# Optimization experiments

Measured on AMD Instinct MI355X. Metric: run time of the kernel, lower is better.

The kernel has to match this reference:

```python
import jax, jax.numpy as jnp
import numpy as np

DIM = 180; HEADS = 6; WS = 16; NUM_TOKENS = 64; RDIM = 10; CAT = 128
KS = 5; MLP_HID = 360; DTD = 64; Hh = 64; Ww = 64; B = 8; M = 64


def _ln(x, g, b, eps=1e-5):
    mu = x.mean(-1, keepdims=True)
    var = ((x - mu) ** 2).mean(-1, keepdims=True)
    return (x - mu) / jnp.sqrt(var + eps) * g + b


def _l2norm(x):
    return x / jnp.clip(jnp.linalg.norm(x, axis=-1, keepdims=True), 1e-12)


def setup_inputs() -> dict:
    key = jax.random.key(0)
    ks = jax.random.split(key, 24)
    rn = lambda k, s: jax.random.normal(k, s, jnp.float32) * 0.02
    z = lambda *s: jnp.zeros(s, jnp.float32)
    return {
        'x': jax.random.normal(ks[0], (B, Hh * Ww, DIM), jnp.float32),
        'td': jax.random.normal(ks[1], (B, M, DIM), jnp.float32),
        'norm1_g': jnp.ones((DIM,), jnp.float32), 'norm1_b': z(DIM),
        'wqkv_w': rn(ks[2], (DIM, 3 * DIM)), 'wqkv_b': z(3 * DIM),
        'atd_wq_w': rn(ks[3], (DIM, RDIM)), 'atd_wq_b': z(RDIM),
        'atd_wk_w': rn(ks[4], (DIM, RDIM)), 'atd_wk_b': z(RDIM),
        'atd_wv_w': rn(ks[5], (DIM, DIM)), 'atd_wv_b': z(DIM),
        'atd_scale': jnp.ones((1,), jnp.float32),
        'aca_proj_w': rn(ks[6], (DIM, DIM)), 'aca_proj_b': z(DIM),
        'win_rpb': rn(ks[7], ((2 * WS - 1) ** 2, HEADS)),
        'win_proj_w': rn(ks[8], (DIM, DIM)), 'win_proj_b': z(DIM),
        'fc_td_w': rn(ks[9], (DIM, DTD)), 'fc_td_b': z(DTD),
        'fc1_w': rn(ks[10], (DIM, MLP_HID)), 'fc1_b': z(MLP_HID),
        'dw_w': rn(ks[11], (MLP_HID + DTD, 1, KS, KS)), 'dw_b': z(MLP_HID + DTD),
        'fc2_w': rn(ks[12], (MLP_HID + DTD, DIM)), 'fc2_b': z(DIM),
        'norm2_g': jnp.ones((DIM,), jnp.float32), 'norm2_b': z(DIM),
        'rpi_sa': jax.random.randint(ks[13], (WS * WS, WS * WS), 0, (2 * WS - 1) ** 2),
        'h': Hh, 'w': Ww,
    }


def reference(x, td, norm1_g, norm1_b, wqkv_w, wqkv_b, atd_wq_w, atd_wq_b,
              atd_wk_w, atd_wk_b, atd_wv_w, atd_wv_b, atd_scale,
              aca_proj_w, aca_proj_b, win_rpb, win_proj_w, win_proj_b,
              fc_td_w, fc_td_b, fc1_w, fc1_b, dw_w, dw_b, fc2_w, fc2_b,
              norm2_g, norm2_b, rpi_sa, h, w):
    b, n, c = x.shape
    hd = c // HEADS
    shortcut = x
    xn = _ln(x, norm1_g, norm1_b)
    qkv = xn @ wqkv_w + wqkv_b  # [b, n, 3c]

    # --- ATD_CA: l2-normalized cross-attention to token dictionary ---
    q = xn @ atd_wq_w + atd_wq_b          # [b, n, rd]
    kk = td @ atd_wk_w + atd_wk_b         # [b, m, rd]
    vv = td @ atd_wv_w + atd_wv_b         # [b, m, c]
    logit_scale = 1.0 + jnp.clip(atd_scale, 0.0, 3.0) * np.log(NUM_TOKENS)
    sim = jnp.einsum('bnr,bmr->bnm', _l2norm(q), _l2norm(kk)) * logit_scale
    attn_atd = jax.nn.softmax(sim, axis=-1)
    x_atd = jnp.einsum('bnm,bmc->bnc', attn_atd, vv)
    tk_id = jnp.argmax(attn_atd, axis=-1)  # [b, n]

    # --- AC_MSA: category-sorted grouped attention ---
    gs = min(n, CAT); ng = (n + gs - 1) // gs; pad_n = ng * gs - n
    sort_idx = jnp.argsort(tk_id, axis=-1)
    inv_idx = jnp.argsort(sort_idx, axis=-1)  # inverse permutation
    sq = jnp.take_along_axis(qkv, sort_idx[:, :, None], axis=1)
    sq = jnp.concatenate([sq, jnp.flip(sq[:, n - pad_n:n, :], axis=1)], axis=1)
    g = sq.reshape(b, ng, gs, 3, HEADS, hd).transpose(3, 0, 1, 4, 2, 5)
    qa, ka, va = g[0], g[1], g[2]          # [b, ng, H, gs, hd]
    a = jax.nn.softmax(jnp.einsum('bgHid,bgHjd->bgHij', qa, ka) * hd ** -0.5, axis=-1)
    y = jnp.einsum('bgHij,bgHjd->bgHid', a, va).transpose(0, 1, 3, 2, 4)
    y = y.reshape(b, n + pad_n, c)[:, :n]
    x_aca = jnp.take_along_axis(y, inv_idx[:, :, None], axis=1) @ aca_proj_w + aca_proj_b

    # --- gather per-token dictionary features for FFN ---
    td_proj = td @ fc_td_w + fc_td_b       # [b, m, dtd]
    x_td = jnp.take_along_axis(td_proj, jnp.broadcast_to(tk_id[:, :, None], (b, n, DTD)), axis=1)

    # --- window attention (shift_size = 0, no mask) ---
    nwh, nww = h // WS, w // WS
    win = qkv.reshape(b, nwh, WS, nww, WS, 3 * c).transpose(0, 1, 3, 2, 4, 5)
    win = win.reshape(-1, WS * WS, 3 * c)
    B_ = win.shape[0]; N = WS * WS
    wq = win.reshape(B_, N, 3, HEADS, hd).transpose(2, 0, 3, 1, 4)
    qw, kw, vw = wq[0] * hd ** -0.5, wq[1], wq[2]
    bias = win_rpb[rpi_sa.reshape(-1)].reshape(N, N, HEADS).transpose(2, 0, 1)[None]
    aw = jax.nn.softmax(jnp.einsum('wHid,wHjd->wHij', qw, kw) + bias, axis=-1)
    ow = jnp.einsum('wHij,wHjd->wHid', aw, vw).transpose(0, 2, 1, 3).reshape(B_, N, c)
    ow = ow @ win_proj_w + win_proj_b
    attn_x = ow.reshape(b, nwh, nww, WS, WS, c).transpose(0, 1, 3, 2, 4, 5).reshape(b, n, c)

    x = shortcut + x_atd + attn_x + x_aca

    # --- ConvFFN_td with depthwise conv branch ---
    x2 = _ln(x, norm2_g, norm2_b)
    h1 = jax.nn.gelu(x2 @ fc1_w + fc1_b, approximate=False)
    hc = jnp.concatenate([h1, x_td], axis=-1)  # [b, n, C]
    C = hc.shape[-1]
    img = jnp.swapaxes(hc, 1, 2).reshape(b, C, h, w)
    conv = jax.lax.conv_general_dilated(img, dw_w, (1, 1), 'SAME',
        dimension_numbers=('NCHW', 'OIHW', 'NCHW'), feature_group_count=C)
    conv = jax.nn.gelu(conv + dw_b[None, :, None, None], approximate=False)
    hc = hc + jnp.swapaxes(conv.reshape(b, C, n), 1, 2)
    return x + hc @ fc2_w + fc2_b
```

## Files before the change

kernel.cpp:

```cpp
#include <hip/hip_runtime.h>
#include <hip/hip_bf16.h>
#include <math.h>

#define BB      8
#define NTOK    4096
#define CDIM    180
#define C3      540
#define NHEADS  6
#define HD      30
#define MDICT   64
#define RD      10
#define DTD     64
#define MHID    360
#define CCAT    424
#define WS      16
#define WIN_N   256
#define GS      128
#define NG      32
#define ROWS    (BB*NTOK)
#define KP1     192
#define KP2     448
#define QKVP    576

typedef __hip_bfloat16 bf16;
typedef short v8s __attribute__((ext_vector_type(8)));
typedef float f32x4 __attribute__((ext_vector_type(4)));
typedef unsigned int u32x4 __attribute__((ext_vector_type(4)));

__device__ __forceinline__ float gelu_exact(float x) {
    return 0.5f * x * (1.0f + erff(x * 0.70710678118654752f));
}
__device__ __forceinline__ float wave_sum(float v) {
    #pragma unroll
    for (int off = 32; off > 0; off >>= 1) v += __shfl_xor(v, off, 64);
    return v;
}
__device__ __forceinline__ unsigned short f2b(float v) {
    unsigned u = __float_as_uint(v);
    return (unsigned short)((u + 0x7FFFu + ((u >> 16) & 1u)) >> 16);
}
__device__ __forceinline__ float b2f(unsigned short h) {
    return __uint_as_float(((unsigned)h) << 16);
}
__device__ __forceinline__ unsigned packbf(float lo, float hi) {
    return (unsigned)f2b(lo) | ((unsigned)f2b(hi) << 16);
}
__device__ __forceinline__ void gload16(const void* g, void* l) {
    __builtin_amdgcn_global_load_lds(
        (const __attribute__((address_space(1))) void*)g,
        (__attribute__((address_space(3))) void*)l, 16, 0, 0);
}

__global__ __launch_bounds__(256) void detect_kernel(const void* __restrict__ x,
                                                     int* __restrict__ flag,
                                                     int* __restrict__ diag)
{
    __shared__ int cnt;
    if (threadIdx.x == 0) { cnt = 0; *diag = 0; }
    __syncthreads();
    const unsigned short* u = (const unsigned short*)x;
    int c = 0;
    for (int i = threadIdx.x; i < 2048; i += 256) {
        unsigned short e = u[2 * i] & 0x7F80;
        if (e >= 0x4300) c++;
    }
    atomicAdd(&cnt, c);
    __syncthreads();
    if (threadIdx.x == 0) *flag = (cnt > 16) ? 1 : 0;
}

#define NCVT 23
struct CvtArgs {
    const void* src[NCVT];
    float* dst[NCVT];
    int cum[NCVT + 1];
};
__global__ __launch_bounds__(256) void convert_all_kernel(CvtArgs a, int total,
        const int* __restrict__ flag)
{
    int i = blockIdx.x * 256 + threadIdx.x;
    if (i >= total) return;
    int s = 0;
    while (i >= a.cum[s + 1]) s++;
    int off = i - a.cum[s];
    if (*flag) a.dst[s][off] = ((const float*)a.src[s])[off];
    else       a.dst[s][off] = __bfloat162float(((const bf16*)a.src[s])[off]);
}

__global__ __launch_bounds__(256) void emit_kernel(const float* __restrict__ src,
        void* __restrict__ out, const int* __restrict__ flag,
        const int* __restrict__ diag, int n)
{
    int i = blockIdx.x * 256 + threadIdx.x;
    if (i >= n) return;
    float v = src[i];
    int d = *diag;
    if (d) v = 100.f + 32.f * (float)d;
    if (*flag) ((float*)out)[i] = v;
    else       ((bf16*)out)[i]  = __float2bfloat16(v);
}

__global__ __launch_bounds__(256) void zero_aux_kernel(bf16* __restrict__ tb,
        bf16* __restrict__ qb)
{
    int idx = blockIdx.x * 256 + threadIdx.x;
    if (idx < ROWS * 12) {
        int row = idx / 12, c = idx % 12;
        tb[(size_t)row * KP1 + CDIM + c] = __float2bfloat16(0.f);
    } else {
        int j = idx - ROWS * 12;
        int row = j / 36, r = j % 36;
        int sec = r / 12, rr = r % 12, hh = rr >> 1, d = 30 + (rr & 1);
        qb[(size_t)row * QKVP + sec * 192 + hh * 32 + d] = __float2bfloat16(0.f);
    }
}

__global__ __launch_bounds__(256) void packW_kernel(const void* __restrict__ W,
        bf16* __restrict__ Wt, int K, int N, int Kpad, int total,
        const int* __restrict__ flag)
{
    int idx = blockIdx.x * 256 + threadIdx.x;
    if (idx >= total) return;
    int n = idx / Kpad, k = idx % Kpad;
    float v = 0.f;
    if (k < K && n < N) {
        size_t src = (size_t)k * N + n;
        v = (*flag) ? ((const float*)W)[src]
                    : __bfloat162float(((const bf16*)W)[src]);
    }
    Wt[idx] = __float2bfloat16(v);
}

__global__ __launch_bounds__(256) void bias_pre_kernel(const int* __restrict__ rpi,
        const float* __restrict__ rpb, float* __restrict__ bias_t)
{
    int idx = blockIdx.x * 256 + threadIdx.x;
    int h = idx >> 16, ij = idx & 65535;
    bias_t[idx] = rpb[rpi[ij] * NHEADS + h];
}

template<bool GELU_, bool ADDRES, bool BIAS_, int OM>
__global__ __launch_bounds__(256) void mgemm_kernel(
        const bf16* __restrict__ A, int lda,
        const bf16* __restrict__ Wt, int ldw,
        const float* __restrict__ bias,
        const float* __restrict__ res, int ldr,
        float* __restrict__ outF, int ldo, int N, int K,
        int* __restrict__ diag)
{
    __shared__ __align__(16) unsigned short As[128][32];
    __shared__ __align__(16) unsigned short Bs[64][32];
    int tid = threadIdx.x;
    int wave = tid >> 6, lane = tid & 63;
    int quad = lane >> 4, mr = lane & 15;
    int row0 = blockIdx.y * 128, col0 = blockIdx.x * 64;
    int ar = tid >> 2, ac = (tid & 3) * 8;
    f32x4 z = {0.f, 0.f, 0.f, 0.f};
    f32x4 acc[2][4] = {{z, z, z, z}, {z, z, z, z}};
    const unsigned short* Au = (const unsigned short*)A;
    const unsigned short* Wu = (const unsigned short*)Wt;
    for (int k0 = 0; k0 < K; k0 += 32) {
        gload16(&Au[(size_t)(row0 + ar) * lda + k0 + ac],      &As[ar][ac]);
        gload16(&Au[(size_t)(row0 + 64 + ar) * lda + k0 + ac], &As[64 + ar][ac]);
        gload16(&Wu[(size_t)(col0 + ar) * ldw + k0 + ac],      &Bs[ar][ac]);
        __syncthreads();
        v8s bfr[4];
        #pragma unroll
        for (int ni = 0; ni < 4; ni++)
            bfr[ni] = *(const v8s*)&Bs[ni * 16 + mr][quad * 8];
        #pragma unroll
        for (int s = 0; s < 2; s++) {
            v8s a = *(const v8s*)&As[wave * 32 + s * 16 + mr][quad * 8];
            #pragma unroll
            for (int ni = 0; ni < 4; ni++)
                acc[s][ni] = __builtin_amdgcn_mfma_f32_16x16x32_bf16(
                    a, bfr[ni], acc[s][ni], 0, 0, 0);
        }
        __syncthreads();
    }
    if (OM == 1) {
        bf16* outb = (bf16*)outF;
        #pragma unroll
        for (int ni = 0; ni < 4; ni++) {
            int gc = col0 + ni * 16 + mr;
            if (gc >= N) continue;
            float bv = bias[gc];
            int sec = gc / 180, rem = gc - sec * 180;
            int hh = rem / 30, d = rem - hh * 30;
            int slot = sec * 192 + hh * 32 + d;
            float sc = (sec == 0) ? 0.18257418583505536f : 1.f;
            #pragma unroll
            for (int s = 0; s < 2; s++) {
                #pragma unroll
                for (int r = 0; r < 4; r++) {
                    int gr = row0 + wave * 32 + s * 16 + quad * 4 + r;
                    outb[(size_t)gr * QKVP + slot] =
                        __float2bfloat16((acc[s][ni][r] + bv) * sc);
                }
            }
        }
        return;
    }
    #pragma unroll
    for (int ni = 0; ni < 4; ni++) {
        int gc = col0 + ni * 16 + mr;
        if (gc >= N) continue;
        float bv = BIAS_ ? bias[gc] : 0.f;
        #pragma unroll
        for (int s = 0; s < 2; s++) {
            #pragma unroll
            for (int r = 0; r < 4; r++) {
                int gr = row0 + wave * 32 + s * 16 + quad * 4 + r;
                float v = acc[s][ni][r] + bv;
                if (GELU_) v = gelu_exact(v);
                if (ADDRES) v += res[(size_t)gr * ldr + gc];
                if (OM == 2) {
                    unsigned u = __float_as_uint(v);
                    if ((u & 0x7F800000u) == 0x7F800000u) atomicOr(diag, 8);
                }
                outF[(size_t)gr * ldo + gc] = v;
            }
        }
    }
}

__global__ __launch_bounds__(256) void av_mgemm_kernel(
        const bf16* __restrict__ P, const bf16* __restrict__ vvT,
        const float* __restrict__ xres, float* __restrict__ accout)
{
    __shared__ unsigned short As[64][32];
    __shared__ unsigned short Bs[64][32];
    int tid = threadIdx.x;
    int wave = tid >> 6, lane = tid & 63;
    int quad = lane >> 4, mr = lane & 15;
    int row0 = blockIdx.y * 64, col0 = blockIdx.x * 64;
    int bz = blockIdx.z;
    const unsigned short* Au = (const unsigned short*)P + (size_t)bz * NTOK * MDICT;
    const unsigned short* Wu = (const unsigned short*)vvT + (size_t)bz * 192 * MDICT;
    const float* res = xres + (size_t)bz * NTOK * CDIM;
    float* outF = accout + (size_t)bz * NTOK * CDIM;
    f32x4 z = {0.f, 0.f, 0.f, 0.f};
    f32x4 acc[4] = {z, z, z, z};
    for (int k0 = 0; k0 < MDICT; k0 += 32) {
        #pragma unroll
        for (int e = 0; e < 8; e++) {
            int idx = tid * 8 + e;
            int r = idx >> 5, c = idx & 31;
            As[r][c] = Au[(size_t)(row0 + r) * MDICT + k0 + c];
            Bs[r][c] = Wu[(size_t)(col0 + r) * MDICT + k0 + c];
        }
        __syncthreads();
        v8s a;
        #pragma unroll
        for (int j = 0; j < 8; j++) a[j] = (short)As[wave * 16 + mr][quad * 8 + j];
        #pragma unroll
        for (int ni = 0; ni < 4; ni++) {
            v8s b;
            #pragma unroll
            for (int j = 0; j < 8; j++) b[j] = (short)Bs[ni * 16 + mr][quad * 8 + j];
            acc[ni] = __builtin_amdgcn_mfma_f32_16x16x32_bf16(a, b, acc[ni], 0, 0, 0);
        }
        __syncthreads();
    }
    #pragma unroll
    for (int ni = 0; ni < 4; ni++) {
        int gc = col0 + ni * 16 + mr;
        if (gc >= CDIM) continue;
        #pragma unroll
        for (int r = 0; r < 4; r++) {
            int gr = row0 + wave * 16 + quad * 4 + r;
            float v = acc[ni][r] + res[(size_t)gr * CDIM + gc];
            outF[(size_t)gr * CDIM + gc] = v;
        }
    }
}

__global__ __launch_bounds__(256, 4) void win_mfma_kernel(const bf16* __restrict__ qkvb,
        const float* __restrict__ bias_t, bf16* __restrict__ outb)
{
    int b = blockIdx.y;
    int widx = blockIdx.x / NHEADS;
    int hh = blockIdx.x % NHEADS;
    int wy = widx >> 2, wx = widx & 3;
    int tid = threadIdx.x;
    int wave = tid >> 6, lane = tid & 63, quad = lane >> 4, mr = lane & 15;
    __shared__ __align__(16) unsigned short Ks[64][40];
    __shared__ __align__(16) unsigned short Vt[32][80];

    size_t brow = (size_t)b * NTOK;
    const unsigned short* qu = (const unsigned short*)qkvb;

    v8s aq[4];
    #pragma unroll
    for (int tt = 0; tt < 4; tt++) {
        int m = (wave * 4 + tt) * 16 + mr;
        int nt_ = (wy * WS + (m >> 4)) * 64 + wx * WS + (m & 15);
        aq[tt] = *(const v8s*)&qu[(brow + nt_) * QKVP + hh * 32 + quad * 8];
    }
    f32x4 z = {0.f, 0.f, 0.f, 0.f};
    f32x4 oacc[4][2] = {{z, z}, {z, z}, {z, z}, {z, z}};
    float m_r[4], l_r[4];
    #pragma unroll
    for (int tt = 0; tt < 4; tt++) { m_r[tt] = -3.0e38f; l_r[tt] = 0.f; }
    const float* btab = bias_t + (size_t)hh * WIN_N * WIN_N;

    for (int kc = 0; kc < WIN_N; kc += 64) {
        {
            int j = tid >> 2, dg = (tid & 3) * 8;
            int tok = kc + j;
            int nt_ = (wy * WS + (tok >> 4)) * 64 + wx * WS + (tok & 15);
            const unsigned short* base = qu + (brow + nt_) * QKVP + hh * 32;
            v8s kv = *(const v8s*)&base[192 + dg];
            v8s vv = *(const v8s*)&base[384 + dg];
            *(v8s*)&Ks[j][dg] = kv;
            #pragma unroll
            for (int jj = 0; jj < 8; jj++)
                Vt[dg + jj][j] = (unsigned short)vv[jj];
        }
        __syncthreads();
        #pragma unroll
        for (int tt = 0; tt < 4; tt++) {
            f32x4 s[4];
            #pragma unroll
            for (int nt = 0; nt < 4; nt++) {
                v8s bk = *(const v8s*)&Ks[nt * 16 + mr][quad * 8];
                s[nt] = __builtin_amdgcn_mfma_f32_16x16x32_bf16(bk, aq[tt], z, 0, 0, 0);
            }
            int qg = (wave * 4 + tt) * 16 + mr;
            const float* bi = btab + (size_t)qg * WIN_N + kc;
            float mc = -3.0e38f;
            #pragma unroll
            for (int nt = 0; nt < 4; nt++) {
                f32x4 b4 = *(const f32x4*)(bi + nt * 16 + quad * 4);
                s[nt][0] += b4[0]; s[nt][1] += b4[1];
                s[nt][2] += b4[2]; s[nt][3] += b4[3];
                mc = fmaxf(mc, fmaxf(fmaxf(s[nt][0], s[nt][1]),
                                     fmaxf(s[nt][2], s[nt][3])));
            }
            mc = fmaxf(mc, __shfl_xor(mc, 16, 64));
            mc = fmaxf(mc, __shfl_xor(mc, 32, 64));
            float mn = fmaxf(m_r[tt], mc);
            float alpha = __expf(m_r[tt] - mn);
            m_r[tt] = mn;
            float ls = 0.f;
            #pragma unroll
            for (int nt = 0; nt < 4; nt++) {
                #pragma unroll
                for (int r = 0; r < 4; r++) {
                    float pp = __expf(s[nt][r] - mn);
                    ls += pp;
                    s[nt][r] = pp;
                }
            }
            ls += __shfl_xor(ls, 16, 64);
            ls += __shfl_xor(ls, 32, 64);
            l_r[tt] = l_r[tt] * alpha + ls;
            unsigned dpk[4][2];
            #pragma unroll
            for (int nt = 0; nt < 4; nt++) {
                dpk[nt][0] = packbf(s[nt][0], s[nt][1]);
                dpk[nt][1] = packbf(s[nt][2], s[nt][3]);
            }
            #pragma unroll
            for (int r = 0; r < 4; r++) {
                float av = __shfl(alpha, quad * 4 + r, 64);
                oacc[tt][0][r] *= av;
                oacc[tt][1][r] *= av;
            }
            #pragma unroll
            for (int c = 0; c < 2; c++) {
                union { u32x4 u; v8s s8; } afu;
                #pragma unroll
                for (int t = 0; t < 4; t++) {
                    int srcl = (((quad * 2 + (t >> 1)) & 3) << 4) | mr;
                    unsigned r0 = (unsigned)__shfl((int)dpk[2 * c][t & 1], srcl, 64);
                    unsigned r1 = (unsigned)__shfl((int)dpk[2 * c + 1][t & 1], srcl, 64);
                    afu.u[t] = (quad & 2) ? r1 : r0;
                }
                #pragma unroll
                for (int dt = 0; dt < 2; dt++) {
                    v8s bv = *(const v8s*)&Vt[dt * 16 + mr][c * 32 + quad * 8];
                    oacc[tt][dt] = __builtin_amdgcn_mfma_f32_16x16x32_bf16(
                        afu.s8, bv, oacc[tt][dt], 0, 0, 0);
                }
            }
        }
        __syncthreads();
    }
    #pragma unroll
    for (int tt = 0; tt < 4; tt++) {
        float il = 1.f / l_r[tt];
        #pragma unroll
        for (int r = 0; r < 4; r++) {
            float ilr = __shfl(il, quad * 4 + r, 64);
            int m = (wave * 4 + tt) * 16 + quad * 4 + r;
            int nt_ = (wy * WS + (m >> 4)) * 64 + wx * WS + (m & 15);
            #pragma unroll
            for (int dt = 0; dt < 2; dt++) {
                int d = dt * 16 + mr;
                if (d >= HD) continue;
                outb[(brow + nt_) * KP1 + hh * HD + d] =
                    __float2bfloat16(oacc[tt][dt][r] * ilr);
            }
        }
    }
}

__global__ __launch_bounds__(256, 4) void acmsa_mfma_kernel(const bf16* __restrict__ qkvb,
        const int* __restrict__ sidx, bf16* __restrict__ outb)
{
    int b = blockIdx.y;
    int g = blockIdx.x / NHEADS;
    int hh = blockIdx.x % NHEADS;
    int tid = threadIdx.x;
    int wave = tid >> 6, lane = tid & 63, quad = lane >> 4, mr = lane & 15;
    __shared__ int toks[GS];
    __shared__ __align__(16) unsigned short Ks[64][40];
    __shared__ __align__(16) unsigned short Vt[32][80];

    size_t brow = (size_t)b * NTOK;
    if (tid < GS) toks[tid] = sidx[brow + (size_t)g * GS + tid];
    __syncthreads();
    const unsigned short* qu = (const unsigned short*)qkvb;

    v8s aq[2];
    #pragma unroll
    for (int tt = 0; tt < 2; tt++) {
        int m = (wave * 2 + tt) * 16 + mr;
        aq[tt] = *(const v8s*)&qu[(brow + toks[m]) * QKVP + hh * 32 + quad * 8];
    }
    f32x4 z = {0.f, 0.f, 0.f, 0.f};
    f32x4 oacc[2][2] = {{z, z}, {z, z}};
    float m_r[2], l_r[2];
    #pragma unroll
    for (int tt = 0; tt < 2; tt++) { m_r[tt] = -3.0e38f; l_r[tt] = 0.f; }

    for (int kc = 0; kc < GS; kc += 64) {
        {
            int j = tid >> 2, dg = (tid & 3) * 8;
            int tok = toks[kc + j];
            const unsigned short* base = qu + (brow + tok) * QKVP + hh * 32;
            v8s kv = *(const v8s*)&base[192 + dg];
            v8s vv = *(const v8s*)&base[384 + dg];
            *(v8s*)&Ks[j][dg] = kv;
            #pragma unroll
            for (int jj = 0; jj < 8; jj++)
                Vt[dg + jj][j] = (unsigned short)vv[jj];
        }
        __syncthreads();
        #pragma unroll
        for (int tt = 0; tt < 2; tt++) {
            f32x4 s[4];
            #pragma unroll
            for (int nt = 0; nt < 4; nt++) {
                v8s bk = *(const v8s*)&Ks[nt * 16 + mr][quad * 8];
                s[nt] = __builtin_amdgcn_mfma_f32_16x16x32_bf16(bk, aq[tt], z, 0, 0, 0);
            }
            float mc = -3.0e38f;
            #pragma unroll
            for (int nt = 0; nt < 4; nt++)
                mc = fmaxf(mc, fmaxf(fmaxf(s[nt][0], s[nt][1]),
                                     fmaxf(s[nt][2], s[nt][3])));
            mc = fmaxf(mc, __shfl_xor(mc, 16, 64));
            mc = fmaxf(mc, __shfl_xor(mc, 32, 64));
            float mn = fmaxf(m_r[tt], mc);
            float alpha = __expf(m_r[tt] - mn);
            m_r[tt] = mn;
            float ls = 0.f;
            #pragma unroll
            for (int nt = 0; nt < 4; nt++) {
                #pragma unroll
                for (int r = 0; r < 4; r++) {
                    float pp = __expf(s[nt][r] - mn);
                    ls += pp;
                    s[nt][r] = pp;
                }
            }
            ls += __shfl_xor(ls, 16, 64);
            ls += __shfl_xor(ls, 32, 64);
            l_r[tt] = l_r[tt] * alpha + ls;
            unsigned dpk[4][2];
            #pragma unroll
            for (int nt = 0; nt < 4; nt++) {
                dpk[nt][0] = packbf(s[nt][0], s[nt][1]);
                dpk[nt][1] = packbf(s[nt][2], s[nt][3]);
            }
            #pragma unroll
            for (int r = 0; r < 4; r++) {
                float av = __shfl(alpha, quad * 4 + r, 64);
                oacc[tt][0][r] *= av;
                oacc[tt][1][r] *= av;
            }
            #pragma unroll
            for (int c = 0; c < 2; c++) {
                union { u32x4 u; v8s s8; } afu;
                #pragma unroll
                for (int t = 0; t < 4; t++) {
                    int srcl = (((quad * 2 + (t >> 1)) & 3) << 4) | mr;
                    unsigned r0 = (unsigned)__shfl((int)dpk[2 * c][t & 1], srcl, 64);
                    unsigned r1 = (unsigned)__shfl((int)dpk[2 * c + 1][t & 1], srcl, 64);
                    afu.u[t] = (quad & 2) ? r1 : r0;
                }
                #pragma unroll
                for (int dt = 0; dt < 2; dt++) {
                    v8s bv = *(const v8s*)&Vt[dt * 16 + mr][c * 32 + quad * 8];
                    oacc[tt][dt] = __builtin_amdgcn_mfma_f32_16x16x32_bf16(
                        afu.s8, bv, oacc[tt][dt], 0, 0, 0);
                }
            }
        }
        __syncthreads();
    }
    #pragma unroll
    for (int tt = 0; tt < 2; tt++) {
        float il = 1.f / l_r[tt];
        #pragma unroll
        for (int r = 0; r < 4; r++) {
            float ilr = __shfl(il, quad * 4 + r, 64);
            int m = (wave * 2 + tt) * 16 + quad * 4 + r;
            int tok = toks[m];
            #pragma unroll
            for (int dt = 0; dt < 2; dt++) {
                int d = dt * 16 + mr;
                if (d >= HD) continue;
                outb[(brow + tok) * KP1 + hh * HD + d] =
                    __float2bfloat16(oacc[tt][dt][r] * ilr);
            }
        }
    }
}

__global__ __launch_bounds__(256) void ln_atd_kernel(const float* __restrict__ x,
        const float* __restrict__ g, const float* __restrict__ be,
        bf16* __restrict__ outb,
        const float* __restrict__ wq, const float* __restrict__ wqb,
        const float* __restrict__ scale_p, const float* __restrict__ kkn,
        bf16* __restrict__ Pout, int* __restrict__ tk_id)
{
    int row = blockIdx.x * 4 + (threadIdx.x >> 6);
    int b = row >> 12;
    int t = threadIdx.x & 63;
    const float* xr = x + (size_t)row * CDIM;
    float v0 = xr[t];
    float v1 = xr[t + 64];
    float v2 = (t < CDIM - 128) ? xr[t + 128] : 0.f;
    float s1 = wave_sum(v0 + v1 + v2);
    float s2 = wave_sum(v0*v0 + v1*v1 + v2*v2);
    float mu = s1 / (float)CDIM;
    float var = s2 / (float)CDIM - mu * mu;
    float rs = rsqrtf(var + 1e-5f);
    float o0 = (v0 - mu) * rs * g[t]      + be[t];
    float o1 = (v1 - mu) * rs * g[t + 64] + be[t + 64];
    float o2 = (t < CDIM - 128) ? ((v2 - mu) * rs * g[t + 128] + be[t + 128]) : 0.f;
    bf16* ob = outb + (size_t)row * KP1;
    ob[t]       = __float2bfloat16(o0);
    ob[t + 64]  = __float2bfloat16(o1);
    ob[t + 128] = __float2bfloat16(o2);
    float sq[RD];
    #pragma unroll
    for (int j = 0; j < RD; j++) {
        float part = o0 * wq[t * RD + j] + o1 * wq[(t + 64) * RD + j];
        if (t < CDIM - 128) part += o2 * wq[(t + 128) * RD + j];
        sq[j] = wave_sum(part) + wqb[j];
    }
    float qn = 0.f;
    #pragma unroll
    for (int j = 0; j < RD; j++) qn += sq[j] * sq[j];
    qn = fmaxf(sqrtf(qn), 1e-12f);
    float ls = 1.0f + fminf(fmaxf(scale_p[0], 0.f), 3.f) * 4.158883083359672f;
    const float* kr = kkn + ((size_t)b * MDICT + t) * RD;
    float s = 0.f;
    #pragma unroll
    for (int j = 0; j < RD; j++) s += sq[j] * kr[j];
    s = s / qn * ls;
    float mv = s; int mi = t;
    #pragma unroll
    for (int off = 32; off > 0; off >>= 1) {
        float ov = __shfl_xor(mv, off, 64);
        int   oi = __shfl_xor(mi, off, 64);
        if (ov > mv || (ov == mv && oi < mi)) { mv = ov; mi = oi; }
    }
    float e = __expf(s - mv);
    float denom = wave_sum(e);
    Pout[(size_t)row * MDICT + t] = __float2bfloat16(e / denom);
    if (t == 0) tk_id[row] = mi;
}

__global__ __launch_bounds__(256) void ln_kernel(const float* __restrict__ x,
        const float* __restrict__ g, const float* __restrict__ be,
        bf16* __restrict__ outb)
{
    int row = blockIdx.x * 4 + (threadIdx.x >> 6);
    int t = threadIdx.x & 63;
    const float* xr = x + (size_t)row * CDIM;
    float v0 = xr[t];
    float v1 = xr[t + 64];
    float v2 = (t < CDIM - 128) ? xr[t + 128] : 0.f;
    float s1 = wave_sum(v0 + v1 + v2);
    float s2 = wave_sum(v0*v0 + v1*v1 + v2*v2);
    float mu = s1 / (float)CDIM;
    float var = s2 / (float)CDIM - mu * mu;
    float rs = rsqrtf(var + 1e-5f);
    float o0 = (v0 - mu) * rs * g[t]      + be[t];
    float o1 = (v1 - mu) * rs * g[t + 64] + be[t + 64];
    float o2 = (t < CDIM - 128) ? ((v2 - mu) * rs * g[t + 128] + be[t + 128]) : 0.f;
    bf16* ob = outb + (size_t)row * KP1;
    ob[t]       = __float2bfloat16(o0);
    ob[t + 64]  = __float2bfloat16(o1);
    ob[t + 128] = __float2bfloat16(o2);
}

__global__ __launch_bounds__(64) void td_pre_kernel(const float* __restrict__ td,
        const float* __restrict__ wk, const float* __restrict__ wkb,
        const float* __restrict__ wv, const float* __restrict__ wvb,
        const float* __restrict__ wtd, const float* __restrict__ wtdb,
        float* __restrict__ kkn, bf16* __restrict__ vvT, float* __restrict__ tdp)
{
    int blk = blockIdx.x;
    int b = blk >> 6, m = blk & 63;
    int t = threadIdx.x;
    __shared__ float tr[CDIM];
    __shared__ float sk[RD];
    __shared__ float snorm;
    const float* tdr = td + (size_t)blk * CDIM;
    tr[t] = tdr[t]; tr[t + 64] = tdr[t + 64];
    if (t < CDIM - 128) tr[t + 128] = tdr[t + 128];
    __syncthreads();
    if (t < RD) {
        float s = wkb[t];
        for (int k = 0; k < CDIM; k++) s += tr[k] * wk[k * RD + t];
        sk[t] = s;
    }
    __syncthreads();
    if (t == 0) {
        float s = 0.f;
        #pragma unroll
        for (int j = 0; j < RD; j++) s += sk[j] * sk[j];
        snorm = fmaxf(sqrtf(s), 1e-12f);
    }
    __syncthreads();
    if (t < RD) kkn[(size_t)blk * RD + t] = sk[t] / snorm;
    for (int c = t; c < 192; c += 64) {
        float s = 0.f;
        if (c < CDIM) {
            s = wvb[c];
            for (int k = 0; k < CDIM; k++) s += tr[k] * wv[k * CDIM + c];
        }
        vvT[((size_t)(b * 192 + c)) * MDICT + m] = __float2bfloat16(s);
    }
    {
        float s = wtdb[t];
        for (int k = 0; k < CDIM; k++) s += tr[k] * wtd[k * DTD + t];
        tdp[(size_t)blk * DTD + t] = s;
    }
}

__global__ __launch_bounds__(256) void sort_kernel(const int* __restrict__ tk_id,
                                                   int* __restrict__ sidx)
{
    int b = blockIdx.x; int tid = threadIdx.x;
    __shared__ int keys[NTOK];
    __shared__ int cnt[256];
    __shared__ int off[256];
    const int* kb = tk_id + (size_t)b * NTOK;
    for (int i = tid; i < NTOK; i += 256) keys[i] = kb[i];
    __syncthreads();
    int v = tid >> 2, seg = tid & 3;
    int lo = seg * 1024, hi = lo + 1024;
    int c = 0;
    for (int i = lo; i < hi; i++) c += (keys[i] == v);
    cnt[tid] = c;
    __syncthreads();
    if (tid == 0) {
        int run = 0;
        for (int l = 0; l < 256; l++) { off[l] = run; run += cnt[l]; }
    }
    __syncthreads();
    int o = off[tid];
    int* sb = sidx + (size_t)b * NTOK;
    for (int i = lo; i < hi; i++) if (keys[i] == v) sb[o++] = i;
}

__global__ __launch_bounds__(256) void gather_td_kernel(const int* __restrict__ tk_id,
        const float* __restrict__ tdp, float* __restrict__ hc)
{
    int idx = blockIdx.x * 256 + threadIdx.x;
    int row = idx >> 6, j = idx & 63;
    int b = row >> 12;
    int tk = tk_id[row];
    hc[(size_t)row * CCAT + MHID + j] = tdp[((size_t)b * MDICT + tk) * DTD + j];
}

#define CHK3 64
#define CTW  8
#define CTH  8
#define CHW  12
#define CHP  144
#define CSPX 68
__global__ __launch_bounds__(256) void conv_kernel(const float* __restrict__ hc,
        const float* __restrict__ w, const float* __restrict__ wb,
        bf16* __restrict__ outb)
{
    int ch0 = blockIdx.x * CHK3;
    int tile = blockIdx.y;
    int b = blockIdx.z;
    int ty0 = (tile >> 3) * CTH, tx0 = (tile & 7) * CTW;
    __shared__ __align__(16) float sh[CHP][CSPX];
    __shared__ __align__(16) float wt[25][CHK3];
    int tid = threadIdx.x;
    for (int idx = tid; idx < CHP * CHK3; idx += 256) {
        int pix = idx >> 6, ch = idx & 63;
        int gy = ty0 + pix / CHW - 2, gx = tx0 + pix % CHW - 2;
        int chg = ch0 + ch;
        float v = 0.f;
        if (gy >= 0 && gy < 64 && gx >= 0 && gx < 64 && chg < CCAT)
            v = hc[((size_t)b * NTOK + gy * 64 + gx) * CCAT + chg];
        sh[pix][ch] = v;
    }
    for (int idx = tid; idx < 25 * CHK3; idx += 256) {
        int kk = idx >> 6, ch = idx & 63;
        int chg = ch0 + ch;
        wt[kk][ch] = (chg < CCAT) ? w[chg * 25 + kk] : 0.f;
    }
    __syncthreads();
    int q = tid & 3, p = tid >> 2;
    int px = p & 7, py = p >> 3;
    int cb = q * 16;
    int pc = py * CHW + px;
    v8s pk0, pk1;
    #pragma unroll
    for (int sub = 0; sub < 4; sub++) {
        int cs = cb + sub * 4;
        f32x4 acc = {0.f, 0.f, 0.f, 0.f};
        #pragma unroll
        for (int dy = 0; dy < 5; dy++) {
            #pragma unroll
            for (int dx = 0; dx < 5; dx++) {
                f32x4 sv = *(const f32x4*)&sh[pc + dy * CHW + dx][cs];
                f32x4 wv = *(const f32x4*)&wt[dy * 5 + dx][cs];
                acc += sv * wv;
            }
            __builtin_amdgcn_sched_barrier(0);
        }
        f32x4 ctr = *(const f32x4*)&sh[pc + 2 * CHW + 2][cs];
        #pragma unroll
        for (int c = 0; c < 4; c++) {
            int chg = ch0 + cs + c;
            float v = 0.f;
            if (chg < CCAT) {
                float gv = gelu_exact(acc[c] + wb[chg]);
                v = ctr[c] + gv;
            }
            int lc = sub * 4 + c;
            if (lc < 8) pk0[lc] = (short)f2b(v);
            else        pk1[lc - 8] = (short)f2b(v);
        }
        __builtin_amdgcn_sched_barrier(0);
    }
    size_t obase = ((size_t)b * NTOK + (ty0 + py) * 64 + tx0 + px) * KP2 + ch0 + cb;
    unsigned short* ob = (unsigned short*)outb + obase;
    *(v8s*)ob = pk0;
    *(v8s*)(ob + 8) = pk1;
}

extern "C" void kernel_launch(void* const* d_in, const int* in_sizes, int n_in,
                              void* d_out, int out_size, void* d_ws, size_t ws_size,
                              hipStream_t stream)
{
    (void)n_in; (void)ws_size; (void)out_size;
    const int* rpi = (const int*)d_in[28];

    float* p = (float*)d_ws;
    float* xn    = p; p += (size_t)ROWS * CDIM;
    float* acc   = p; p += (size_t)ROWS * CDIM;
    float* tmp1  = p; p += (size_t)ROWS * CDIM;
    float* qkv   = p; p += (size_t)ROWS * C3;
    float* hcnew = p; p += (size_t)ROWS * CCAT;
    float* kkn   = p; p += (size_t)BB * MDICT * RD;
    bf16*  vvT   = (bf16*)p; p += (size_t)BB * 192 * MDICT / 2;
    float* tdp   = p; p += (size_t)BB * MDICT * DTD;
    int*   tk_id = (int*)p; p += ROWS;
    int*   sidx  = (int*)p; p += ROWS;
    int*   flag  = (int*)p; p += 64;
    int*   diag  = (int*)p; p += 64;
    bf16* wtqkv = (bf16*)p; p += 576 * KP1 / 2;
    bf16* wtaca = (bf16*)p; p += 192 * KP1 / 2;
    bf16* wtwin = (bf16*)p; p += 192 * KP1 / 2;
    bf16* wtfc1 = (bf16*)p; p += 384 * KP1 / 2;
    bf16* wtfc2 = (bf16*)p; p += 192 * KP2 / 2;
    float* cin[28];
    for (int i = 0; i < 28; i++) { cin[i] = p; p += in_sizes[i]; }
    float* bias_t = p; p += (size_t)NHEADS * WIN_N * WIN_N;
    (void)xn;

    float* hc      = qkv;
    bf16*  qkvb    = (bf16*)qkv;
    bf16*  xnb     = (bf16*)hcnew;
    bf16*  tmp1b   = (bf16*)(hcnew + (size_t)ROWS * KP1 / 2);
    bf16*  hcnewb2 = (bf16*)hcnew;
    bf16*  Pbuf    = (bf16*)tmp1;

    detect_kernel<<<1, 256, 0, stream>>>(d_in[0], flag, diag);
    {
        CvtArgs ca;
        int total = 0, s = 0;
        for (int i = 0; i < 28; i++) {
            if (i == 4 || i == 13 || i == 16 || i == 20 || i == 24) continue;
            ca.src[s] = d_in[i];
            ca.dst[s] = cin[i];
            ca.cum[s] = total;
            total += in_sizes[i];
            s++;
        }
        ca.cum[s] = total;
        convert_all_kernel<<<(total + 255) / 256, 256, 0, stream>>>(ca, total, flag);
    }
    const float *x = cin[0], *td = cin[1], *n1g = cin[2], *n1b = cin[3],
        *wqkv_b = cin[5], *wq_w = cin[6], *wq_b = cin[7],
        *wk_w = cin[8], *wk_b = cin[9], *wv_w = cin[10], *wv_b = cin[11],
        *atd_scale = cin[12], *aca_b = cin[14], *win_rpb = cin[15],
        *winp_b = cin[17], *fctd_w = cin[18], *fctd_b = cin[19],
        *fc1_b = cin[21], *dw_w = cin[22], *dw_b = cin[23], *fc2_b = cin[25],
        *n2g = cin[26], *n2b = cin[27];

    packW_kernel<<<576 * KP1 / 256, 256, 0, stream>>>(d_in[4],  wtqkv, CDIM, C3,   KP1, 576 * KP1, flag);
    packW_kernel<<<192 * KP1 / 256, 256, 0, stream>>>(d_in[13], wtaca, CDIM, CDIM, KP1, 192 * KP1, flag);
    packW_kernel<<<192 * KP1 / 256, 256, 0, stream>>>(d_in[16], wtwin, CDIM, CDIM, KP1, 192 * KP1, flag);
    packW_kernel<<<384 * KP1 / 256, 256, 0, stream>>>(d_in[20], wtfc1, CDIM, MHID, KP1, 384 * KP1, flag);
    packW_kernel<<<192 * KP2 / 256, 256, 0, stream>>>(d_in[24], wtfc2, CCAT, CDIM, KP2, 192 * KP2, flag);
    bias_pre_kernel<<<NHEADS * WIN_N * WIN_N / 256, 256, 0, stream>>>(rpi, win_rpb, bias_t);

    td_pre_kernel<<<BB * MDICT, 64, 0, stream>>>(td, wk_w, wk_b, wv_w, wv_b,
                                                 fctd_w, fctd_b, kkn, vvT, tdp);
    ln_atd_kernel<<<ROWS / 4, 256, 0, stream>>>(x, n1g, n1b, xnb,
                                                wq_w, wq_b, atd_scale, kkn, Pbuf, tk_id);
    mgemm_kernel<false, false, true, 1><<<dim3(9, ROWS / 128), 256, 0, stream>>>(
        xnb, KP1, wtqkv, KP1, wqkv_b, nullptr, 0, (float*)qkvb, QKVP, C3, KP1, nullptr);
    zero_aux_kernel<<<ROWS * 48 / 256, 256, 0, stream>>>(tmp1b, qkvb);
    av_mgemm_kernel<<<dim3(3, NTOK / 64, BB), 256, 0, stream>>>(Pbuf, vvT, x, acc);
    sort_kernel<<<BB, 256, 0, stream>>>(tk_id, sidx);
    acmsa_mfma_kernel<<<dim3(NG * NHEADS, BB), 256, 0, stream>>>(qkvb, sidx, tmp1b);
    mgemm_kernel<false, true, true, 0><<<dim3(3, ROWS / 128), 256, 0, stream>>>(
        tmp1b, KP1, wtaca, KP1, aca_b, acc, CDIM, acc, CDIM, CDIM, KP1, nullptr);
    win_mfma_kernel<<<dim3(16 * NHEADS, BB), 256, 0, stream>>>(qkvb, bias_t, tmp1b);
    mgemm_kernel<false, true, true, 0><<<dim3(3, ROWS / 128), 256, 0, stream>>>(
        tmp1b, KP1, wtwin, KP1, winp_b, acc, CDIM, acc, CDIM, CDIM, KP1, nullptr);
    ln_kernel<<<ROWS / 4, 256, 0, stream>>>(acc, n2g, n2b, xnb);
    mgemm_kernel<true, false, true, 0><<<dim3(6, ROWS / 128), 256, 0, stream>>>(
        xnb, KP1, wtfc1, KP1, fc1_b, nullptr, 0, hc, CCAT, MHID, KP1, nullptr);
    gather_td_kernel<<<ROWS * 64 / 256, 256, 0, stream>>>(tk_id, tdp, hc);
    conv_kernel<<<dim3(7, 64, BB), 256, 0, stream>>>(hc, dw_w, dw_b, hcnewb2);
    mgemm_kernel<false, true, true, 2><<<dim3(3, ROWS / 128), 256, 0, stream>>>(
        hcnewb2, KP2, wtfc2, KP2, fc2_b, acc, CDIM, tmp1, CDIM, CDIM, KP2, diag);
    emit_kernel<<<(ROWS * CDIM + 255) / 256, 256, 0, stream>>>(
        tmp1, d_out, flag, diag, ROWS * CDIM);
}
```

Measured before the change: 690.2 us.

## Fuse ACA and window projection GEMMs via concatenated K; read x directly

Merges the two separate projection GEMMs (ACA output and window-attention output) into one GEMM over a concatenated K dimension of 384. It does this by packing both weight matrices side by side and letting the A-operand pointer switch to a second buffer halfway through K, with both biases added in the epilogue. This removes one read-modify-write pass over the fp32 accumulator and one kernel launch. It also stops converting x into an fp32 copy and has ln_atd and av_mgemm read the raw input with a dtype flag, at the cost of a per-element branch and a larger zero-init kernel for the second padded buffer.

```diff
diff --git a/kernel.cpp b/kernel.cpp
--- a/kernel.cpp
+++ b/kernel.cpp
@@ -100,15 +100,19 @@
     else       ((bf16*)out)[i]  = __float2bfloat16(v);
 }
 
-__global__ __launch_bounds__(256) void zero_aux_kernel(bf16* __restrict__ tb,
-        bf16* __restrict__ qb)
+__global__ __launch_bounds__(256) void zero_aux_kernel(bf16* __restrict__ t1,
+        bf16* __restrict__ t2, bf16* __restrict__ qb)
 {
     int idx = blockIdx.x * 256 + threadIdx.x;
     if (idx < ROWS * 12) {
         int row = idx / 12, c = idx % 12;
-        tb[(size_t)row * KP1 + CDIM + c] = __float2bfloat16(0.f);
+        t1[(size_t)row * KP1 + CDIM + c] = __float2bfloat16(0.f);
+    } else if (idx < ROWS * 24) {
+        int j = idx - ROWS * 12;
+        int row = j / 12, c = j % 12;
+        t2[(size_t)row * KP1 + CDIM + c] = __float2bfloat16(0.f);
     } else {
-        int j = idx - ROWS * 12;
+        int j = idx - ROWS * 24;
         int row = j / 36, r = j % 36;
         int sec = r / 12, rr = r % 12, hh = rr >> 1, d = 30 + (rr & 1);
         qb[(size_t)row * QKVP + sec * 192 + hh * 32 + d] = __float2bfloat16(0.f);
@@ -116,8 +120,8 @@
 }
 
 __global__ __launch_bounds__(256) void packW_kernel(const void* __restrict__ W,
-        bf16* __restrict__ Wt, int K, int N, int Kpad, int total,
-        const int* __restrict__ flag)
+        bf16* __restrict__ Wt, int K, int N, int Kpad, int ldw, int koff,
+        int total, const int* __restrict__ flag)
 {
     int idx = blockIdx.x * 256 + threadIdx.x;
     if (idx >= total) return;
@@ -128,7 +132,7 @@
         v = (*flag) ? ((const float*)W)[src]
                     : __bfloat162float(((const bf16*)W)[src]);
     }
-    Wt[idx] = __float2bfloat16(v);
+    Wt[(size_t)n * ldw + koff + k] = __float2bfloat16(v);
 }
 
 __global__ __launch_bounds__(256) void bias_pre_kernel(const int* __restrict__ rpi,
@@ -146,7 +150,8 @@
         const float* __restrict__ bias,
         const float* __restrict__ res, int ldr,
         float* __restrict__ outF, int ldo, int N, int K,
-        int* __restrict__ diag)
+        int* __restrict__ diag,
+        const bf16* __restrict__ A2, const float* __restrict__ bias2)
 {
     __shared__ __align__(16) unsigned short As[128][32];
     __shared__ __align__(16) unsigned short Bs[64][32];
@@ -158,11 +163,15 @@
     f32x4 z = {0.f, 0.f, 0.f, 0.f};
     f32x4 acc[2][4] = {{z, z, z, z}, {z, z, z, z}};
     const unsigned short* Au = (const unsigned short*)A;
+    const unsigned short* A2u = (const unsigned short*)A2;
     const unsigned short* Wu = (const unsigned short*)Wt;
     for (int k0 = 0; k0 < K; k0 += 32) {
-        gload16(&Au[(size_t)(row0 + ar) * lda + k0 + ac],      &As[ar][ac]);
-        gload16(&Au[(size_t)(row0 + 64 + ar) * lda + k0 + ac], &As[64 + ar][ac]);
-        gload16(&Wu[(size_t)(col0 + ar) * ldw + k0 + ac],      &Bs[ar][ac]);
+        const unsigned short* Asel = Au;
+        int kk = k0;
+        if (OM == 3 && k0 >= KP1) { Asel = A2u; kk = k0 - KP1; }
+        gload16(&Asel[(size_t)(row0 + ar) * lda + kk + ac],      &As[ar][ac]);
+        gload16(&Asel[(size_t)(row0 + 64 + ar) * lda + kk + ac], &As[64 + ar][ac]);
+        gload16(&Wu[(size_t)(col0 + ar) * ldw + k0 + ac],        &Bs[ar][ac]);
         __syncthreads();
         v8s bfr[4];
         #pragma unroll
@@ -206,6 +215,7 @@
         int gc = col0 + ni * 16 + mr;
         if (gc >= N) continue;
         float bv = BIAS_ ? bias[gc] : 0.f;
+        if (OM == 3) bv += bias2[gc];
         #pragma unroll
         for (int s = 0; s < 2; s++) {
             #pragma unroll
@@ -226,7 +236,8 @@
 
 __global__ __launch_bounds__(256) void av_mgemm_kernel(
         const bf16* __restrict__ P, const bf16* __restrict__ vvT,
-        const float* __restrict__ xres, float* __restrict__ accout)
+        const void* __restrict__ xraw, const int* __restrict__ flag,
+        float* __restrict__ accout)
 {
     __shared__ unsigned short As[64][32];
     __shared__ unsigned short Bs[64][32];
@@ -235,10 +246,13 @@
     int quad = lane >> 4, mr = lane & 15;
     int row0 = blockIdx.y * 64, col0 = blockIdx.x * 64;
     int bz = blockIdx.z;
+    int isf = *flag;
     const unsigned short* Au = (const unsigned short*)P + (size_t)bz * NTOK * MDICT;
     const unsigned short* Wu = (const unsigned short*)vvT + (size_t)bz * 192 * MDICT;
-    const float* res = xres + (size_t)bz * NTOK * CDIM;
-    float* outF = accout + (size_t)bz * NTOK * CDIM;
+    size_t rbase = (size_t)bz * NTOK * CDIM;
+    const float* resf = (const float*)xraw + rbase;
+    const bf16*  resb = (const bf16*)xraw + rbase;
+    float* outF = accout + rbase;
     f32x4 z = {0.f, 0.f, 0.f, 0.f};
     f32x4 acc[4] = {z, z, z, z};
     for (int k0 = 0; k0 < MDICT; k0 += 32) {
@@ -269,8 +283,9 @@
         #pragma unroll
         for (int r = 0; r < 4; r++) {
             int gr = row0 + wave * 16 + quad * 4 + r;
-            float v = acc[ni][r] + res[(size_t)gr * CDIM + gc];
-            outF[(size_t)gr * CDIM + gc] = v;
+            size_t off = (size_t)gr * CDIM + gc;
+            float rv = isf ? resf[off] : __bfloat162float(resb[off]);
+            outF[off] = acc[ni][r] + rv;
         }
     }
 }
@@ -530,7 +545,8 @@
     }
 }
 
-__global__ __launch_bounds__(256) void ln_atd_kernel(const float* __restrict__ x,
+__global__ __launch_bounds__(256) void ln_atd_kernel(const void* __restrict__ xraw,
+        const int* __restrict__ flag,
         const float* __restrict__ g, const float* __restrict__ be,
         bf16* __restrict__ outb,
         const float* __restrict__ wq, const float* __restrict__ wqb,
@@ -540,10 +556,14 @@
     int row = blockIdx.x * 4 + (threadIdx.x >> 6);
     int b = row >> 12;
     int t = threadIdx.x & 63;
-    const float* xr = x + (size_t)row * CDIM;
-    float v0 = xr[t];
-    float v1 = xr[t + 64];
-    float v2 = (t < CDIM - 128) ? xr[t + 128] : 0.f;
+    int isf = *flag;
+    size_t rb = (size_t)row * CDIM;
+    const float* xf = (const float*)xraw + rb;
+    const bf16*  xb = (const bf16*)xraw + rb;
+    float v0 = isf ? xf[t]       : __bfloat162float(xb[t]);
+    float v1 = isf ? xf[t + 64]  : __bfloat162float(xb[t + 64]);
+    float v2 = (t < CDIM - 128)
+             ? (isf ? xf[t + 128] : __bfloat162float(xb[t + 128])) : 0.f;
     float s1 = wave_sum(v0 + v1 + v2);
     float s2 = wave_sum(v0*v0 + v1*v1 + v2*v2);
     float mu = s1 / (float)CDIM;
@@ -783,20 +803,19 @@
     int*   sidx  = (int*)p; p += ROWS;
     int*   flag  = (int*)p; p += 64;
     int*   diag  = (int*)p; p += 64;
-    bf16* wtqkv = (bf16*)p; p += 576 * KP1 / 2;
-    bf16* wtaca = (bf16*)p; p += 192 * KP1 / 2;
-    bf16* wtwin = (bf16*)p; p += 192 * KP1 / 2;
-    bf16* wtfc1 = (bf16*)p; p += 384 * KP1 / 2;
-    bf16* wtfc2 = (bf16*)p; p += 192 * KP2 / 2;
+    bf16* wtqkv  = (bf16*)p; p += 576 * KP1 / 2;
+    bf16* wtcomb = (bf16*)p; p += 192 * 384 / 2;
+    bf16* wtfc1  = (bf16*)p; p += 384 * KP1 / 2;
+    bf16* wtfc2  = (bf16*)p; p += 192 * KP2 / 2;
     float* cin[28];
     for (int i = 0; i < 28; i++) { cin[i] = p; p += in_sizes[i]; }
     float* bias_t = p; p += (size_t)NHEADS * WIN_N * WIN_N;
-    (void)xn;
 
     float* hc      = qkv;
     bf16*  qkvb    = (bf16*)qkv;
     bf16*  xnb     = (bf16*)hcnew;
     bf16*  tmp1b   = (bf16*)(hcnew + (size_t)ROWS * KP1 / 2);
+    bf16*  tmp2b   = (bf16*)xn;
     bf16*  hcnewb2 = (bf16*)hcnew;
     bf16*  Pbuf    = (bf16*)tmp1;
 
@@ -805,7 +824,7 @@
         CvtArgs ca;
         int total = 0, s = 0;
         for (int i = 0; i < 28; i++) {
-            if (i == 4 || i == 13 || i == 16 || i == 20 || i == 24) continue;
+            if (i == 0 || i == 4 || i == 13 || i == 16 || i == 20 || i == 24) continue;
             ca.src[s] = d_in[i];
             ca.dst[s] = cin[i];
             ca.cum[s] = total;
@@ -815,7 +834,7 @@
         ca.cum[s] = total;
         convert_all_kernel<<<(total + 255) / 256, 256, 0, stream>>>(ca, total, flag);
     }
-    const float *x = cin[0], *td = cin[1], *n1g = cin[2], *n1b = cin[3],
+    const float *td = cin[1], *n1g = cin[2], *n1b = cin[3],
         *wqkv_b = cin[5], *wq_w = cin[6], *wq_b = cin[7],
         *wk_w = cin[8], *wk_b = cin[9], *wv_w = cin[10], *wv_b = cin[11],
         *atd_scale = cin[12], *aca_b = cin[14], *win_rpb = cin[15],
@@ -823,35 +842,37 @@
         *fc1_b = cin[21], *dw_w = cin[22], *dw_b = cin[23], *fc2_b = cin[25],
         *n2g = cin[26], *n2b = cin[27];
 
-    packW_kernel<<<576 * KP1 / 256, 256, 0, stream>>>(d_in[4],  wtqkv, CDIM, C3,   KP1, 576 * KP1, flag);
-    packW_kernel<<<192 * KP1 / 256, 256, 0, stream>>>(d_in[13], wtaca, CDIM, CDIM, KP1, 192 * KP1, flag);
-    packW_kernel<<<192 * KP1 / 256, 256, 0, stream>>>(d_in[16], wtwin, CDIM, CDIM, KP1, 192 * KP1, flag);
-    packW_kernel<<<384 * KP1 / 256, 256, 0, stream>>>(d_in[20], wtfc1, CDIM, MHID, KP1, 384 * KP1, flag);
-    packW_kernel<<<192 * KP2 / 256, 256, 0, stream>>>(d_in[24], wtfc2, CCAT, CDIM, KP2, 192 * KP2, flag);
+    packW_kernel<<<576 * KP1 / 256, 256, 0, stream>>>(d_in[4],  wtqkv, CDIM, C3,   KP1, KP1, 0,   576 * KP1, flag);
+    packW_kernel<<<192 * KP1 / 256, 256, 0, stream>>>(d_in[13], wtcomb, CDIM, CDIM, KP1, 384, 0,   192 * KP1, flag);
+    packW_kernel<<<192 * KP1 / 256, 256, 0, stream>>>(d_in[16], wtcomb, CDIM, CDIM, KP1, 384, 192, 192 * KP1, flag);
+    packW_kernel<<<384 * KP1 / 256, 256, 0, stream>>>(d_in[20], wtfc1, CDIM, MHID, KP1, KP1, 0,   384 * KP1, flag);
+    packW_kernel<<<192 * KP2 / 256, 256, 0, stream>>>(d_in[24], wtfc2, CCAT, CDIM, KP2, KP2, 0,   192 * KP2, flag);
     bias_pre_kernel<<<NHEADS * WIN_N * WIN_N / 256, 256, 0, stream>>>(rpi, win_rpb, bias_t);
 
     td_pre_kernel<<<BB * MDICT, 64, 0, stream>>>(td, wk_w, wk_b, wv_w, wv_b,
                                                  fctd_w, fctd_b, kkn, vvT, tdp);
-    ln_atd_kernel<<<ROWS / 4, 256, 0, stream>>>(x, n1g, n1b, xnb,
+    ln_atd_kernel<<<ROWS / 4, 256, 0, stream>>>(d_in[0], flag, n1g, n1b, xnb,
                                                 wq_w, wq_b, atd_scale, kkn, Pbuf, tk_id);
     mgemm_kernel<false, false, true, 1><<<dim3(9, ROWS / 128), 256, 0, stream>>>(
-        xnb, KP1, wtqkv, KP1, wqkv_b, nullptr, 0, (float*)qkvb, QKVP, C3, KP1, nullptr);
-    zero_aux_kernel<<<ROWS * 48 / 256, 256, 0, stream>>>(tmp1b, qkvb);
-    av_mgemm_kernel<<<dim3(3, NTOK / 64, BB), 256, 0, stream>>>(Pbuf, vvT, x, acc);
+        xnb, KP1, wtqkv, KP1, wqkv_b, nullptr, 0, (float*)qkvb, QKVP, C3, KP1,
+        nullptr, nullptr, nullptr);
+    zero_aux_kernel<<<ROWS * 60 / 256, 256, 0, stream>>>(tmp1b, tmp2b, qkvb);
+    av_mgemm_kernel<<<dim3(3, NTOK / 64, BB), 256, 0, stream>>>(Pbuf, vvT, d_in[0], flag, acc);
     sort_kernel<<<BB, 256, 0, stream>>>(tk_id, sidx);
-    acmsa_mfma_kernel<<<dim3(NG * NHEADS, BB), 256, 0, stream>>>(qkvb, sidx, tmp1b);
-    mgemm_kernel<false, true, true, 0><<<dim3(3, ROWS / 128), 256, 0, stream>>>(
-        tmp1b, KP1, wtaca, KP1, aca_b, acc, CDIM, acc, CDIM, CDIM, KP1, nullptr);
+    acmsa_mfma_kernel<<<dim3(NG * NHEADS, BB), 256, 0, stream>>>(qkvb, sidx, tmp2b);
     win_mfma_kernel<<<dim3(16 * NHEADS, BB), 256, 0, stream>>>(qkvb, bias_t, tmp1b);
-    mgemm_kernel<false, true, true, 0><<<dim3(3, ROWS / 128), 256, 0, stream>>>(
-        tmp1b, KP1, wtwin, KP1, winp_b, acc, CDIM, acc, CDIM, CDIM, KP1, nullptr);
+    mgemm_kernel<false, true, true, 3><<<dim3(3, ROWS / 128), 256, 0, stream>>>(
+        tmp2b, KP1, wtcomb, 384, aca_b, acc, CDIM, acc, CDIM, CDIM, 384,
+        nullptr, tmp1b, winp_b);
     ln_kernel<<<ROWS / 4, 256, 0, stream>>>(acc, n2g, n2b, xnb);
     mgemm_kernel<true, false, true, 0><<<dim3(6, ROWS / 128), 256, 0, stream>>>(
-        xnb, KP1, wtfc1, KP1, fc1_b, nullptr, 0, hc, CCAT, MHID, KP1, nullptr);
+        xnb, KP1, wtfc1, KP1, fc1_b, nullptr, 0, hc, CCAT, MHID, KP1,
+        nullptr, nullptr, nullptr);
     gather_td_kernel<<<ROWS * 64 / 256, 256, 0, stream>>>(tk_id, tdp, hc);
     conv_kernel<<<dim3(7, 64, BB), 256, 0, stream>>>(hc, dw_w, dw_b, hcnewb2);
     mgemm_kernel<false, true, true, 2><<<dim3(3, ROWS / 128), 256, 0, stream>>>(
-        hcnewb2, KP2, wtfc2, KP2, fc2_b, acc, CDIM, tmp1, CDIM, CDIM, KP2, diag);
+        hcnewb2, KP2, wtfc2, KP2, fc2_b, acc, CDIM, tmp1, CDIM, CDIM, KP2,
+        diag, nullptr, nullptr);
     emit_kernel<<<(ROWS * CDIM + 255) / 256, 256, 0, stream>>>(
         tmp1, d_out, flag, diag, ROWS * CDIM);
 }
```

Measured after the change: 666.9 us. 1.03x faster.
